# Optimization experiments

Hardware: AMD Instinct MI355X
Metric: run time of the kernel (lower is better)

## Reference

```python
import jax, jax.numpy as jnp
import numpy as np
import math

B, T, D, H = 4, 2048, 1024, 16
ND = D // H  # head dim = 64


def setup_inputs() -> dict:
    key = jax.random.key(0)
    ks = jax.random.split(key, 12)
    s = 1.0 / math.sqrt(D)
    inp = {
        "q": jax.random.normal(ks[0], (B, T, D), jnp.float32),
        "k": jax.random.normal(ks[1], (B, T, D), jnp.float32),
        "v": jax.random.normal(ks[2], (B, T, D), jnp.float32),
        # nn.Linear params: weight [out,in], bias [out]
        "wq": jax.random.normal(ks[3], (D, D), jnp.float32) * s,
        "bq": jax.random.normal(ks[4], (D,), jnp.float32) * s,
        "wk": jax.random.normal(ks[5], (D, D), jnp.float32) * s,
        "bk": jax.random.normal(ks[6], (D,), jnp.float32) * s,
        "wv": jax.random.normal(ks[7], (D, D), jnp.float32) * s,
        "bv": jax.random.normal(ks[8], (D,), jnp.float32) * s,
        "wo": jax.random.normal(ks[9], (D, D), jnp.float32) * s,
        "bo": jax.random.normal(ks[10], (D,), jnp.float32) * s,
        # causal mask: 1 where attending allowed, 0 -> -inf
        "mask": jnp.tril(jnp.ones((T, T), jnp.int32)),
    }
    return inp


def reference(q, k, v, wq, bq, wk, bk, wv, bv, wo, bo, mask):
    batch, time, dim = q.shape
    n_d = dim // H
    # NOTE: original module (faithfully reproduced bug) computes k and v from q
    Q = q @ wq.T + bq
    K = q @ wk.T + bk
    V = q @ wv.T + bv
    # [B, T, D] -> [B, H, T, nd]
    Q = Q.reshape(batch, time, H, n_d).transpose(0, 2, 1, 3)
    K = K.reshape(batch, time, H, n_d).transpose(0, 2, 1, 3)
    V = V.reshape(batch, time, H, n_d).transpose(0, 2, 1, 3)
    score = jnp.einsum("bhqd,bhkd->bhqk", Q, K) / math.sqrt(n_d)
    score = jnp.where(mask == 0, -jnp.inf, score)
    # original uses nn.Softmax(dim=-2): normalize over the QUERY axis
    attn = jax.nn.softmax(score, axis=-2)
    out = jnp.einsum("bhqk,bhkd->bhqd", attn, V)
    out = out.transpose(0, 2, 1, 3).reshape(batch, time, dim)
    return out @ wo.T + bo
```

## Files before the change

### kernel.cpp

```cpp
#include <hip/hip_runtime.h>
#include <stdint.h>

#define B_  4
#define T_  2048
#define D_  1024
#define H_  16
#define ND_ 64
#define M_  (B_ * T_)

typedef unsigned short u16;
typedef __bf16 bf8  __attribute__((ext_vector_type(8)));
typedef float  f4   __attribute__((ext_vector_type(4)));
typedef u16    u16x8 __attribute__((ext_vector_type(8)));

__device__ inline u16 f2bf(float f) {
    unsigned int x = __builtin_bit_cast(unsigned int, f);
    x += 0x7fffu + ((x >> 16) & 1u);
    return (u16)(x >> 16);
}
__device__ inline unsigned int cvt_pk_bf16(float a, float b) {
    unsigned int r;
    asm("v_cvt_pk_bf16_f32 %0, %1, %2" : "=v"(r) : "v"(a), "v"(b));
    return r;
}
__device__ inline f4 mfma16(bf8 a, bf8 b, f4 c) {
    return __builtin_amdgcn_mfma_f32_16x16x32_bf16(a, b, c, 0, 0, 0);
}
__device__ inline void async16(const void* g, void* l) {
    auto gp = reinterpret_cast<const __attribute__((address_space(1))) unsigned int*>(
        reinterpret_cast<uintptr_t>(g));
    auto lp = reinterpret_cast<__attribute__((address_space(3))) unsigned int*>(
        reinterpret_cast<uintptr_t>(l));
    __builtin_amdgcn_global_load_lds(gp, lp, 16, 0, 0);
}

__global__ __launch_bounds__(256)
void cvt_bf16(const float* __restrict__ in, u16* __restrict__ out, int n) {
    int i = (blockIdx.x * blockDim.x + threadIdx.x) * 8;
    if (i + 8 <= n) {
        float4 a = *(const float4*)(in + i);
        float4 b = *(const float4*)(in + i + 4);
        u16x8 o;
        o[0] = f2bf(a.x); o[1] = f2bf(a.y); o[2] = f2bf(a.z); o[3] = f2bf(a.w);
        o[4] = f2bf(b.x); o[5] = f2bf(b.y); o[6] = f2bf(b.z); o[7] = f2bf(b.w);
        *(u16x8*)(out + i) = o;
    }
}

__global__ __launch_bounds__(256)
void cvt_w4(const float* __restrict__ w0, const float* __restrict__ w1,
            const float* __restrict__ w2, const float* __restrict__ w3,
            u16* __restrict__ o0, u16* __restrict__ o1,
            u16* __restrict__ o2, u16* __restrict__ o3) {
    const float* in; u16* out;
    switch (blockIdx.y) {
        case 0:  in = w0; out = o0; break;
        case 1:  in = w1; out = o1; break;
        case 2:  in = w2; out = o2; break;
        default: in = w3; out = o3; break;
    }
    int i = (blockIdx.x * blockDim.x + threadIdx.x) * 8;
    float4 a = *(const float4*)(in + i);
    float4 b = *(const float4*)(in + i + 4);
    u16x8 o;
    o[0] = f2bf(a.x); o[1] = f2bf(a.y); o[2] = f2bf(a.z); o[3] = f2bf(a.w);
    o[4] = f2bf(b.x); o[5] = f2bf(b.y); o[6] = f2bf(b.z); o[7] = f2bf(b.w);
    *(u16x8*)(out + i) = o;
}

__global__ __launch_bounds__(256, 2)
void gemm_qkv(const u16* __restrict__ A, const u16* __restrict__ W,
              const float* __restrict__ bq, const float* __restrict__ bk,
              const float* __restrict__ bvp,
              u16* __restrict__ Qh, u16* __restrict__ Kh, u16* __restrict__ Vtr) {
    constexpr int K = 1024;
    __shared__ __attribute__((aligned(16))) u16 sA[2][128 * 32];
    __shared__ __attribute__((aligned(16))) u16 sB[2][128 * 32];
    const int tid  = threadIdx.x;
    const int wave = tid >> 6;
    const int lane = tid & 63;
    const int m0 = blockIdx.y * 128;
    const int n0 = blockIdx.x * 128;
    const int wm = (wave & 1) * 64;
    const int wn = (wave >> 1) * 64;

    f4 acc[4][4] = {};

    const int srow = wave * 32 + (lane >> 2);
    const int scol = (lane & 3) * 8;
    const u16* gA = A + (size_t)(m0 + srow) * K + scol;
    const u16* gB = W + (size_t)(n0 + srow) * K + scol;
    const int lo0 = (wave * 32) * 32;
    const int lo1 = (wave * 32 + 16) * 32;

    const int row = lane & 15;
    const int qo  = (lane >> 4) * 8;

    async16(gA, sA[0] + lo0);
    async16(gA + (size_t)16 * K, sA[0] + lo1);
    async16(gB, sB[0] + lo0);
    async16(gB + (size_t)16 * K, sB[0] + lo1);
    __syncthreads();

    int p = 0;
    for (int k0 = 0; k0 < K; k0 += 32) {
        const int kn = k0 + 32;
        if (kn < K) {
            async16(gA + kn, sA[p ^ 1] + lo0);
            async16(gA + kn + (size_t)16 * K, sA[p ^ 1] + lo1);
            async16(gB + kn, sB[p ^ 1] + lo0);
            async16(gB + kn + (size_t)16 * K, sB[p ^ 1] + lo1);
        }
        bf8 af[4], bfr[4];
#pragma unroll
        for (int i = 0; i < 4; i++)
            af[i] = *(const bf8*)(sA[p] + (wm + i * 16 + row) * 32 + qo);
#pragma unroll
        for (int i = 0; i < 4; i++)
            bfr[i] = *(const bf8*)(sB[p] + (wn + i * 16 + row) * 32 + qo);
#pragma unroll
        for (int mi = 0; mi < 4; mi++)
#pragma unroll
            for (int ni = 0; ni < 4; ni++)
                acc[mi][ni] = mfma16(af[mi], bfr[ni], acc[mi][ni]);
        __syncthreads();
        p ^= 1;
    }

    const int which = n0 >> 10;
    const float* bias = which == 0 ? bq : (which == 1 ? bk : bvp);
    u16* outQK = which == 0 ? Qh : Kh;

#pragma unroll
    for (int ni = 0; ni < 4; ni++) {
        const int n  = n0 + wn + ni * 16 + row;
        const int nl = n & 1023;
        const float bvv = bias[nl];
#pragma unroll
        for (int mi = 0; mi < 4; mi++) {
#pragma unroll
            for (int r = 0; r < 4; r++) {
                const int m = m0 + wm + mi * 16 + (lane >> 4) * 4 + r;
                float v = acc[mi][ni][r] + bvv;
                if (which == 0) v *= 0.125f;
                if (which < 2) {
                    size_t idx = (((size_t)((m >> 11) * H_ + (nl >> 6)) * T_) + (m & (T_ - 1))) * ND_ +
                                 (nl & (ND_ - 1));
                    outQK[idx] = f2bf(v);
                } else {
                    size_t idx = ((size_t)(((m >> 11) * H_ + (nl >> 6)) * ND_ + (nl & (ND_ - 1)))) * T_ +
                                 (m & (T_ - 1));
                    Vtr[idx] = f2bf(v);
                }
            }
        }
    }
}

__global__ __launch_bounds__(256, 2)
void gemm_out(const u16* __restrict__ A, const u16* __restrict__ W,
              const float* __restrict__ bias, float* __restrict__ Cout) {
    constexpr int K = 1024;
    constexpr int N = 1024;
    __shared__ __attribute__((aligned(16))) u16 sA[2][128 * 32];
    __shared__ __attribute__((aligned(16))) u16 sB[2][128 * 32];
    const int tid  = threadIdx.x;
    const int wave = tid >> 6;
    const int lane = tid & 63;
    const int m0 = blockIdx.y * 128;
    const int n0 = blockIdx.x * 128;
    const int wm = (wave & 1) * 64;
    const int wn = (wave >> 1) * 64;

    f4 acc[4][4] = {};

    const int srow = wave * 32 + (lane >> 2);
    const int scol = (lane & 3) * 8;
    const u16* gA = A + (size_t)(m0 + srow) * K + scol;
    const u16* gB = W + (size_t)(n0 + srow) * K + scol;
    const int lo0 = (wave * 32) * 32;
    const int lo1 = (wave * 32 + 16) * 32;

    const int row = lane & 15;
    const int qo  = (lane >> 4) * 8;

    async16(gA, sA[0] + lo0);
    async16(gA + (size_t)16 * K, sA[0] + lo1);
    async16(gB, sB[0] + lo0);
    async16(gB + (size_t)16 * K, sB[0] + lo1);
    __syncthreads();

    int p = 0;
    for (int k0 = 0; k0 < K; k0 += 32) {
        const int kn = k0 + 32;
        if (kn < K) {
            async16(gA + kn, sA[p ^ 1] + lo0);
            async16(gA + kn + (size_t)16 * K, sA[p ^ 1] + lo1);
            async16(gB + kn, sB[p ^ 1] + lo0);
            async16(gB + kn + (size_t)16 * K, sB[p ^ 1] + lo1);
        }
        bf8 af[4], bfr[4];
#pragma unroll
        for (int i = 0; i < 4; i++)
            af[i] = *(const bf8*)(sA[p] + (wm + i * 16 + row) * 32 + qo);
#pragma unroll
        for (int i = 0; i < 4; i++)
            bfr[i] = *(const bf8*)(sB[p] + (wn + i * 16 + row) * 32 + qo);
#pragma unroll
        for (int mi = 0; mi < 4; mi++)
#pragma unroll
            for (int ni = 0; ni < 4; ni++)
                acc[mi][ni] = mfma16(af[mi], bfr[ni], acc[mi][ni]);
        __syncthreads();
        p ^= 1;
    }

#pragma unroll
    for (int ni = 0; ni < 4; ni++) {
        const int n = n0 + wn + ni * 16 + row;
        const float bv = bias[n];
#pragma unroll
        for (int mi = 0; mi < 4; mi++) {
#pragma unroll
            for (int r = 0; r < 4; r++) {
                const int m = m0 + wm + mi * 16 + (lane >> 4) * 4 + r;
                Cout[(size_t)m * N + n] = acc[mi][ni][r] + bv;
            }
        }
    }
}

__global__ __launch_bounds__(256)
void col_sum(const u16* __restrict__ Qh, const u16* __restrict__ Kh,
             float* __restrict__ Ic) {
    __shared__ __attribute__((aligned(16))) u16 sQ[2][32 * 72];
    const int bh   = blockIdx.y;
    const int tid  = threadIdx.x;
    const int wave = tid >> 6;
    const int lane = tid & 63;
    const int l15  = lane & 15;
    const int quad = lane >> 4;
    const int qo   = quad * 8;
    const int sr   = tid >> 3;
    const int sc   = (tid & 7) * 8;
    const u16* Qb = Qh + (size_t)bh * T_ * ND_;
    const u16* Kb = Kh + (size_t)bh * T_ * ND_;

#pragma unroll
    for (int half = 0; half < 2; half++) {
        const int strip = half ? (15 - (int)blockIdx.x) : (int)blockIdx.x;
        const int c0  = strip * 128;
        const int c0w = c0 + wave * 32;
        bf8 b0[2], b1[2];
#pragma unroll
        for (int g = 0; g < 2; g++) {
            b0[g] = *(const bf8*)(Kb + (size_t)(c0w + g * 16 + l15) * ND_ + qo);
            b1[g] = *(const bf8*)(Kb + (size_t)(c0w + g * 16 + l15) * ND_ + 32 + qo);
        }
        float acc[2][4] = {};
        int p = 0;
        u16x8 pq = *(const u16x8*)(Qb + (size_t)(c0 + sr) * ND_ + sc);
        for (int qt = c0; qt < T_; qt += 32) {
            *(u16x8*)(&sQ[p][sr * 72 + sc]) = pq;
            __syncthreads();
            if (qt + 32 < T_)
                pq = *(const u16x8*)(Qb + (size_t)(qt + 32 + sr) * ND_ + sc);
            const bool masked = qt < c0 + 128;
#pragma unroll
            for (int sub = 0; sub < 2; sub++) {
                const int rho = sub * 16 + l15;
                bf8 a0 = *(const bf8*)(&sQ[p][rho * 72 + qo]);
                bf8 a1 = *(const bf8*)(&sQ[p][rho * 72 + 32 + qo]);
#pragma unroll
                for (int g = 0; g < 2; g++) {
                    f4 s = {0.f, 0.f, 0.f, 0.f};
                    s = mfma16(a0, b0[g], s);
                    s = mfma16(a1, b1[g], s);
                    if (masked) {
#pragma unroll
                        for (int r = 0; r < 4; r++) {
                            const int qg = qt + sub * 16 + quad * 4 + r;
                            const int cg = c0w + g * 16 + l15;
                            acc[g][r] += (qg >= cg) ? __expf(s[r]) : 0.f;
                        }
                    } else {
#pragma unroll
                        for (int r = 0; r < 4; r++)
                            acc[g][r] += __expf(s[r]);
                    }
                }
            }
            p ^= 1;
        }
        __syncthreads();
#pragma unroll
        for (int g = 0; g < 2; g++) {
            float l = acc[g][0] + acc[g][1] + acc[g][2] + acc[g][3];
            l += __shfl_xor(l, 16);
            l += __shfl_xor(l, 32);
            if (lane < 16) Ic[(size_t)bh * T_ + c0w + g * 16 + l15] = 1.f / l;
        }
    }
}

__global__ __launch_bounds__(256, 2)
void attn_out(const u16* __restrict__ Qh, const u16* __restrict__ Kh,
              const u16* __restrict__ Vt, const float* __restrict__ Ic,
              u16* __restrict__ AO) {
    __shared__ __attribute__((aligned(16))) u16 sK[64 * 72];
    __shared__ __attribute__((aligned(16))) u16 sVt[64 * 72];
    __shared__ __attribute__((aligned(16))) u16 sP[4][32 * 64];
    const int bh   = blockIdx.x;
    const int b    = bh >> 4;
    const int h    = bh & 15;
    const int tid  = threadIdx.x;
    const int wave = tid >> 6;
    const int lane = tid & 63;
    const int l15  = lane & 15;
    const int quad = lane >> 4;
    const int qo   = quad * 8;
    const int swz  = (l15 & 7) << 4;

    const u16* Qb = Qh + (size_t)bh * T_ * ND_;
    const u16* Kb = Kh + (size_t)bh * T_ * ND_;
    const u16* Vb = Vt + (size_t)bh * ND_ * T_;
    const float* ic = Ic + (size_t)bh * T_;

    const int sr = tid >> 3;
    const int sc = (tid & 7) * 8;
    char* pw = (char*)sP[wave];

#pragma unroll
    for (int half = 0; half < 2; half++) {
        const int jj = half ? (15 - (int)blockIdx.y) : (int)blockIdx.y;
        const int qb = jj * 128;
        const int kend = qb + 128;

        const int qw = qb + wave * 32;
        bf8 aq[2][2];
#pragma unroll
        for (int qs = 0; qs < 2; qs++)
#pragma unroll
            for (int dh = 0; dh < 2; dh++)
                aq[qs][dh] = *(const bf8*)(Qb + (size_t)(qw + qs * 16 + l15) * ND_ + dh * 32 + qo);

        f4 o[2][4] = {};

        u16x8 pk0 = *(const u16x8*)(Kb + (size_t)sr * ND_ + sc);
        u16x8 pk1 = *(const u16x8*)(Kb + (size_t)(sr + 32) * ND_ + sc);
        u16x8 pv0 = *(const u16x8*)(Vb + (size_t)sr * T_ + sc);
        u16x8 pv1 = *(const u16x8*)(Vb + (size_t)(sr + 32) * T_ + sc);

        for (int kt = 0; kt < kend; kt += 64) {
            *(u16x8*)(sK + sr * 72 + sc) = pk0;
            *(u16x8*)(sK + (sr + 32) * 72 + sc) = pk1;
            *(u16x8*)(sVt + sr * 72 + sc) = pv0;
            *(u16x8*)(sVt + (sr + 32) * 72 + sc) = pv1;
            __syncthreads();

            const int ktn = kt + 64;
            if (ktn < kend) {
                pk0 = *(const u16x8*)(Kb + (size_t)(ktn + sr) * ND_ + sc);
                pk1 = *(const u16x8*)(Kb + (size_t)(ktn + sr + 32) * ND_ + sc);
                pv0 = *(const u16x8*)(Vb + (size_t)sr * T_ + ktn + sc);
                pv1 = *(const u16x8*)(Vb + (size_t)(sr + 32) * T_ + ktn + sc);
            }

#pragma unroll
            for (int ks = 0; ks < 4; ks++) {
                bf8 kb0 = *(const bf8*)(sK + (ks * 16 + l15) * 72 + qo);
                bf8 kb1 = *(const bf8*)(sK + (ks * 16 + l15) * 72 + 32 + qo);
                const f4 icv = *(const f4*)(ic + kt + ks * 16 + quad * 4);
                const int kbase = kt + ks * 16 + quad * 4;
#pragma unroll
                for (int qs = 0; qs < 2; qs++) {
                    f4 s = {0.f, 0.f, 0.f, 0.f};
                    s = mfma16(kb0, aq[qs][0], s);
                    s = mfma16(kb1, aq[qs][1], s);
                    f4 p;
                    if (kt + ks * 16 + 15 <= qw + qs * 16) {
#pragma unroll
                        for (int r = 0; r < 4; r++) p[r] = __expf(s[r]) * icv[r];
                    } else {
                        const int qg = qw + qs * 16 + l15;
#pragma unroll
                        for (int r = 0; r < 4; r++)
                            p[r] = (kbase + r <= qg) ? __expf(s[r]) * icv[r] : 0.f;
                    }
                    uint2 w;
                    w.x = cvt_pk_bf16(p[0], p[1]);
                    w.y = cvt_pk_bf16(p[2], p[3]);
                    *(uint2*)(pw + (((qs * 16 + l15) * 128 + ks * 32 + quad * 8) ^ swz)) = w;
                }
            }
#pragma unroll
            for (int st = 0; st < 2; st++) {
                bf8 ap0 = *(const bf8*)(pw + ((l15 * 128 + st * 64 + quad * 16) ^ swz));
                bf8 ap1 = *(const bf8*)(pw + (((16 + l15) * 128 + st * 64 + quad * 16) ^ swz));
#pragma unroll
                for (int ds = 0; ds < 4; ds++) {
                    bf8 bv = *(const bf8*)(sVt + (ds * 16 + l15) * 72 + st * 32 + qo);
                    o[0][ds] = mfma16(ap0, bv, o[0][ds]);
                    o[1][ds] = mfma16(ap1, bv, o[1][ds]);
                }
            }
            __syncthreads();
        }

#pragma unroll
        for (int qs = 0; qs < 2; qs++)
#pragma unroll
            for (int ds = 0; ds < 4; ds++)
#pragma unroll
                for (int r = 0; r < 4; r++) {
                    const int q = qw + qs * 16 + quad * 4 + r;
                    const int d = ds * 16 + l15;
                    AO[((size_t)(b * T_ + q)) * D_ + h * ND_ + d] = f2bf(o[qs][ds][r]);
                }
    }
}

extern "C" void kernel_launch(void* const* d_in, const int* in_sizes, int n_in,
                              void* d_out, int out_size, void* d_ws, size_t ws_size,
                              hipStream_t stream) {
    (void)in_sizes; (void)n_in; (void)out_size; (void)ws_size;
    const float* q  = (const float*)d_in[0];
    const float* wq = (const float*)d_in[3];
    const float* bq = (const float*)d_in[4];
    const float* wk = (const float*)d_in[5];
    const float* bk = (const float*)d_in[6];
    const float* wv = (const float*)d_in[7];
    const float* bv = (const float*)d_in[8];
    const float* wo = (const float*)d_in[9];
    const float* bo = (const float*)d_in[10];

    const size_t SZ = (size_t)M_ * D_;
    const size_t WSZ = (size_t)D_ * D_;
    u16* Qh  = (u16*)d_ws;
    u16* Kh  = Qh + SZ;
    u16* Vtr = Kh + SZ;
    u16* qbf = Vtr + SZ;
    u16* AO  = qbf;
    u16* wqb = qbf + SZ;
    u16* wkb = wqb + WSZ;
    u16* wvb = wkb + WSZ;
    u16* wob = wvb + WSZ;
    float* Ic = (float*)(wob + WSZ);

    cvt_bf16<<<dim3(SZ / 8 / 256), 256, 0, stream>>>(q, qbf, (int)SZ);
    cvt_w4<<<dim3(WSZ / 8 / 256, 4), 256, 0, stream>>>(wq, wk, wv, wo,
                                                       wqb, wkb, wvb, wob);

    dim3 gqkv(3 * D_ / 128, M_ / 128);
    gemm_qkv<<<gqkv, 256, 0, stream>>>(qbf, wqb, bq, bk, bv, Qh, Kh, Vtr);

    dim3 gcs(8, B_ * H_);
    col_sum<<<gcs, 256, 0, stream>>>(Qh, Kh, Ic);

    dim3 ga(B_ * H_, 8);
    attn_out<<<ga, 256, 0, stream>>>(Qh, Kh, Vtr, Ic, AO);

    dim3 gp(D_ / 128, M_ / 128);
    gemm_out<<<gp, 256, 0, stream>>>(AO, wob, bo, (float*)d_out);
}
```

Before: 382.8 us.

## Restructure GEMM double-buffer pipeline with explicit vmcnt waits and two-stage prefetch

Replaces the __syncthreads-based double-buffered K loop in both GEMM kernels with a shared macro. It issues two stages of async global-to-LDS loads up front and waits with s_waitcnt vmcnt(4) so that one stage stays in flight. After the fragments are read into registers it takes a second barrier, then refills the just-consumed buffer before running the MFMAs. The goal is to keep global loads overlapped with compute and to stop the full drain that __syncthreads forces each iteration. In exchange it adds a second barrier per iteration and depends on hand-counted vmcnt values being correct.

Result: no change. 376.9 us (-1.5%).

```diff
diff --git a/kernel.cpp b/kernel.cpp
--- a/kernel.cpp
+++ b/kernel.cpp
@@ -67,6 +67,52 @@
     o[4] = f2bf(b.x); o[5] = f2bf(b.y); o[6] = f2bf(b.z); o[7] = f2bf(b.w);
     *(u16x8*)(out + i) = o;
 }
+
+#define WAIT_VM4()  do { asm volatile("s_waitcnt vmcnt(4)" ::: "memory"); \
+                         __builtin_amdgcn_sched_barrier(0); } while (0)
+#define WAIT_VM0()  do { asm volatile("s_waitcnt vmcnt(0)" ::: "memory"); \
+                         __builtin_amdgcn_sched_barrier(0); } while (0)
+#define WAIT_LGKM() do { asm volatile("s_waitcnt lgkmcnt(0)" ::: "memory"); \
+                         __builtin_amdgcn_sched_barrier(0); } while (0)
+
+#define GEMM_CORE(K)                                                          \
+    async16(gA, sA[0] + lo0);                                                 \
+    async16(gA + (size_t)16 * K, sA[0] + lo1);                                \
+    async16(gB, sB[0] + lo0);                                                 \
+    async16(gB + (size_t)16 * K, sB[0] + lo1);                                \
+    async16(gA + 32, sA[1] + lo0);                                            \
+    async16(gA + 32 + (size_t)16 * K, sA[1] + lo1);                           \
+    async16(gB + 32, sB[1] + lo0);                                            \
+    async16(gB + 32 + (size_t)16 * K, sB[1] + lo1);                           \
+    int p = 0;                                                                \
+    for (int k0 = 0; k0 < K; k0 += 32) {                                      \
+        if (k0 < K - 64) WAIT_VM4(); else WAIT_VM0();                         \
+        __builtin_amdgcn_s_barrier();                                         \
+        __builtin_amdgcn_sched_barrier(0);                                    \
+        bf8 af[4], bfr[4];                                                    \
+        _Pragma("unroll")                                                     \
+        for (int i = 0; i < 4; i++)                                           \
+            af[i] = *(const bf8*)(sA[p] + (wm + i * 16 + row) * 32 + qo);     \
+        _Pragma("unroll")                                                     \
+        for (int i = 0; i < 4; i++)                                           \
+            bfr[i] = *(const bf8*)(sB[p] + (wn + i * 16 + row) * 32 + qo);    \
+        WAIT_LGKM();                                                          \
+        __builtin_amdgcn_s_barrier();                                         \
+        __builtin_amdgcn_sched_barrier(0);                                    \
+        const int kn = k0 + 64;                                               \
+        if (kn < K) {                                                         \
+            async16(gA + kn, sA[p] + lo0);                                    \
+            async16(gA + kn + (size_t)16 * K, sA[p] + lo1);                   \
+            async16(gB + kn, sB[p] + lo0);                                    \
+            async16(gB + kn + (size_t)16 * K, sB[p] + lo1);                   \
+        }                                                                     \
+        _Pragma("unroll")                                                     \
+        for (int mi = 0; mi < 4; mi++)                                        \
+            _Pragma("unroll")                                                 \
+            for (int ni = 0; ni < 4; ni++)                                    \
+                acc[mi][ni] = mfma16(af[mi], bfr[ni], acc[mi][ni]);           \
+        p ^= 1;                                                               \
+    }
 
 __global__ __launch_bounds__(256, 2)
 void gemm_qkv(const u16* __restrict__ A, const u16* __restrict__ W,
@@ -96,36 +142,7 @@
     const int row = lane & 15;
     const int qo  = (lane >> 4) * 8;
 
-    async16(gA, sA[0] + lo0);
-    async16(gA + (size_t)16 * K, sA[0] + lo1);
-    async16(gB, sB[0] + lo0);
-    async16(gB + (size_t)16 * K, sB[0] + lo1);
-    __syncthreads();
-
-    int p = 0;
-    for (int k0 = 0; k0 < K; k0 += 32) {
-        const int kn = k0 + 32;
-        if (kn < K) {
-            async16(gA + kn, sA[p ^ 1] + lo0);
-            async16(gA + kn + (size_t)16 * K, sA[p ^ 1] + lo1);
-            async16(gB + kn, sB[p ^ 1] + lo0);
-            async16(gB + kn + (size_t)16 * K, sB[p ^ 1] + lo1);
-        }
-        bf8 af[4], bfr[4];
-#pragma unroll
-        for (int i = 0; i < 4; i++)
-            af[i] = *(const bf8*)(sA[p] + (wm + i * 16 + row) * 32 + qo);
-#pragma unroll
-        for (int i = 0; i < 4; i++)
-            bfr[i] = *(const bf8*)(sB[p] + (wn + i * 16 + row) * 32 + qo);
-#pragma unroll
-        for (int mi = 0; mi < 4; mi++)
-#pragma unroll
-            for (int ni = 0; ni < 4; ni++)
-                acc[mi][ni] = mfma16(af[mi], bfr[ni], acc[mi][ni]);
-        __syncthreads();
-        p ^= 1;
-    }
+    GEMM_CORE(K)
 
     const int which = n0 >> 10;
     const float* bias = which == 0 ? bq : (which == 1 ? bk : bvp);
@@ -184,36 +201,7 @@
     const int row = lane & 15;
     const int qo  = (lane >> 4) * 8;
 
-    async16(gA, sA[0] + lo0);
-    async16(gA + (size_t)16 * K, sA[0] + lo1);
-    async16(gB, sB[0] + lo0);
-    async16(gB + (size_t)16 * K, sB[0] + lo1);
-    __syncthreads();
-
-    int p = 0;
-    for (int k0 = 0; k0 < K; k0 += 32) {
-        const int kn = k0 + 32;
-        if (kn < K) {
-            async16(gA + kn, sA[p ^ 1] + lo0);
-            async16(gA + kn + (size_t)16 * K, sA[p ^ 1] + lo1);
-            async16(gB + kn, sB[p ^ 1] + lo0);
-            async16(gB + kn + (size_t)16 * K, sB[p ^ 1] + lo1);
-        }
-        bf8 af[4], bfr[4];
-#pragma unroll
-        for (int i = 0; i < 4; i++)
-            af[i] = *(const bf8*)(sA[p] + (wm + i * 16 + row) * 32 + qo);
-#pragma unroll
-        for (int i = 0; i < 4; i++)
-            bfr[i] = *(const bf8*)(sB[p] + (wn + i * 16 + row) * 32 + qo);
-#pragma unroll
-        for (int mi = 0; mi < 4; mi++)
-#pragma unroll
-            for (int ni = 0; ni < 4; ni++)
-                acc[mi][ni] = mfma16(af[mi], bfr[ni], acc[mi][ni]);
-        __syncthreads();
-        p ^= 1;
-    }
+    GEMM_CORE(K)
 
 #pragma unroll
     for (int ni = 0; ni < 4; ni++) {
```
